# Performance work log

Hardware: AMD Instinct MI355X
Metric: run time of the kernel (lower is better)

## Reference

```python
import jax, jax.numpy as jnp
import numpy as np

N = 100000      # nodes
E = 1600000     # edges (avg degree 16)
F_IN = 128      # input feature dim (lazy in_channels=-1)
HID = 256       # hidden_channels
OUT = 128       # out_channels
NCLS = 2        # final softmax classes


def _l2norm(x):
    # F.normalize(p=2, dim=-1) with eps clamp, as SAGEConv(normalize=True)
    n = jnp.linalg.norm(x, axis=-1, keepdims=True)
    return x / jnp.maximum(n, 1e-12)


def _sage(x, src, tgt, Wl, bl, Wr, n_nodes):
    # PyG SAGEConv: mean-aggregate source features at targets, then
    # out = lin_l(mean_aggr) + lin_r(x); lin_l has bias, lin_r does not.
    s = jax.ops.segment_sum(x[src], tgt, num_segments=n_nodes)          # [N, F]
    cnt = jax.ops.segment_sum(jnp.ones((src.shape[0],), x.dtype), tgt,
                              num_segments=n_nodes)                     # [N]
    mean = s / jnp.maximum(cnt, 1.0)[:, None]
    out = mean @ Wl.T + bl + x @ Wr.T
    return _l2norm(out)


def setup_inputs() -> dict:
    key = jax.random.key(0)
    ks = jax.random.split(key, 12)

    def glorot(k, o, i):
        lim = float(np.sqrt(6.0 / (o + i)))
        return jax.random.uniform(k, (o, i), jnp.float32, -lim, lim)

    return {
        "x": jax.random.normal(ks[0], (N, F_IN), jnp.float32),
        "edge_index": jax.random.randint(ks[1], (2, E), 0, N, dtype=jnp.int64),
        # conv1: SAGEConv(F_IN -> HID)
        "W1l": glorot(ks[2], HID, F_IN), "b1l": jnp.zeros((HID,), jnp.float32),
        "W1r": glorot(ks[3], HID, F_IN),
        # linear: HID -> OUT
        "Wlin": glorot(ks[4], OUT, HID), "blin": jnp.zeros((OUT,), jnp.float32),
        # conv2: SAGEConv(OUT -> OUT)
        "W2l": glorot(ks[5], OUT, OUT), "b2l": jnp.zeros((OUT,), jnp.float32),
        "W2r": glorot(ks[6], OUT, OUT),
        # linear2: OUT -> 2
        "Wlin2": glorot(ks[7], NCLS, OUT), "blin2": jnp.zeros((NCLS,), jnp.float32),
    }


def reference(x, edge_index, W1l, b1l, W1r, Wlin, blin, W2l, b2l, W2r, Wlin2, blin2):
    src, tgt = edge_index[0], edge_index[1]
    h = _sage(x, src, tgt, W1l, b1l, W1r, N)            # conv1, normalize
    h = jnp.maximum(h @ Wlin.T + blin, 0.0)             # linear + relu
    y = _sage(h, src, tgt, W2l, b2l, W2r, N)            # conv2, normalize
    logits = y @ Wlin2.T + blin2                        # linear2
    probs = jax.nn.softmax(logits, axis=1)
    return probs, y
```

## Files before the change

kernel.cpp:

```cpp
#include <hip/hip_runtime.h>
#include <hip/hip_bf16.h>
#include <hip/hip_fp8.h>

#define NN   100000
#define NE   1600000
#define NBK  196
#define BSH  9
#define EPB  8192
#define CAP  9216

typedef __attribute__((ext_vector_type(8))) short short8;
typedef __attribute__((ext_vector_type(4))) float f32x4;

__device__ __forceinline__ ushort f2bf(float f) {
    union { float f; uint u; } v; v.f = f;
    uint u = v.u;
    return (ushort)((u + 0x7FFFu + ((u >> 16) & 1u)) >> 16);
}
__device__ __forceinline__ float bf2f(uint b) {
    union { uint u; float f; } v; v.u = b << 16;
    return v.f;
}
__device__ __forceinline__ float fp8f(uint byte) {
    __hip_fp8_e4m3 t; t.__x = (__hip_fp8_storage_t)(byte & 0xffu);
    return (float)t;
}
__device__ __forceinline__ uint f2fp8(float f) {
    __hip_fp8_e4m3 t(f);
    return (uint)t.__x;
}
__device__ __forceinline__ int swz(int off) { return off ^ (((off >> 9) & 7) << 4); }

__global__ __launch_bounds__(256) void bucket_hist(const int* __restrict__ tgt,
                                                   int* __restrict__ bcnt) {
    __shared__ int lh[NBK];
    int tid = threadIdx.x;
    for (int i = tid; i < NBK; i += 256) lh[i] = 0;
    __syncthreads();
    int base4 = blockIdx.x * (EPB / 4);
#pragma unroll
    for (int k = 0; k < 8; ++k) {
        int i4 = base4 + k * 256 + tid;
        if (i4 < NE / 4) {
            int4 t = ((const int4*)tgt)[i4];
            atomicAdd(&lh[t.x >> BSH], 1);
            atomicAdd(&lh[t.y >> BSH], 1);
            atomicAdd(&lh[t.z >> BSH], 1);
            atomicAdd(&lh[t.w >> BSH], 1);
        }
    }
    __syncthreads();
    for (int i = tid; i < NBK; i += 256)
        if (lh[i]) atomicAdd(&bcnt[i], lh[i]);
}

__global__ __launch_bounds__(256) void bucket_scan(const int* __restrict__ bcnt,
                                                   int* __restrict__ bbase,
                                                   int* __restrict__ bcursor,
                                                   int* __restrict__ rowstart) {
    int t = threadIdx.x;
    int v = (t < NBK) ? bcnt[t] : 0;
    int lane = t & 63, wid = t >> 6;
    int inc = v;
#pragma unroll
    for (int off = 1; off < 64; off <<= 1) {
        int u = __shfl_up(inc, off);
        if (lane >= off) inc += u;
    }
    __shared__ int ws[4];
    if (lane == 63) ws[wid] = inc;
    __syncthreads();
    int woff = 0;
    for (int w = 0; w < wid; ++w) woff += ws[w];
    int ex = woff + inc - v;
    if (t < NBK) { bbase[t] = ex; bcursor[t] = ex; }
    if (t == NBK) bbase[NBK] = ex;
    if (t == 255) rowstart[NN] = NE;
}

__global__ __launch_bounds__(256) void bucket_scatter(const int* __restrict__ src,
                                                      const int* __restrict__ tgt,
                                                      int* __restrict__ bcursor,
                                                      uint* __restrict__ brec) {
    __shared__ int lh[NBK + 1];
    __shared__ int lcur[NBK];
    __shared__ int lbase[NBK];
    __shared__ uint lrec[EPB];
    __shared__ int ws[4];
    int tid = threadIdx.x;
    for (int i = tid; i < NBK; i += 256) lh[i] = 0;
    __syncthreads();
    int base4 = blockIdx.x * (EPB / 4);
#pragma unroll
    for (int k = 0; k < 8; ++k) {
        int i4 = base4 + k * 256 + tid;
        if (i4 < NE / 4) {
            int4 t = ((const int4*)tgt)[i4];
            atomicAdd(&lh[t.x >> BSH], 1);
            atomicAdd(&lh[t.y >> BSH], 1);
            atomicAdd(&lh[t.z >> BSH], 1);
            atomicAdd(&lh[t.w >> BSH], 1);
        }
    }
    __syncthreads();
    int v = (tid < NBK) ? lh[tid] : 0;
    int lane = tid & 63, wid = tid >> 6;
    int inc = v;
#pragma unroll
    for (int off = 1; off < 64; off <<= 1) {
        int u = __shfl_up(inc, off);
        if (lane >= off) inc += u;
    }
    if (lane == 63) ws[wid] = inc;
    __syncthreads();
    int woff = 0;
    for (int w = 0; w < wid; ++w) woff += ws[w];
    int ex = woff + inc - v;
    int nval = min(EPB, NE - blockIdx.x * EPB);
    if (tid < NBK) {
        lh[tid] = ex;
        lcur[tid] = ex;
        lbase[tid] = v ? atomicAdd(&bcursor[tid], v) : 0;
    }
    if (tid == 0) lh[NBK] = nval;
    __syncthreads();
#pragma unroll
    for (int k = 0; k < 8; ++k) {
        int i4 = base4 + k * 256 + tid;
        if (i4 < NE / 4) {
            int4 t = ((const int4*)tgt)[i4];
            int4 s = ((const int4*)src)[i4];
            int p;
            p = atomicAdd(&lcur[t.x >> BSH], 1); lrec[p] = ((uint)s.x << BSH) | (uint)(t.x & 511);
            p = atomicAdd(&lcur[t.y >> BSH], 1); lrec[p] = ((uint)s.y << BSH) | (uint)(t.y & 511);
            p = atomicAdd(&lcur[t.z >> BSH], 1); lrec[p] = ((uint)s.z << BSH) | (uint)(t.z & 511);
            p = atomicAdd(&lcur[t.w >> BSH], 1); lrec[p] = ((uint)s.w << BSH) | (uint)(t.w & 511);
        }
    }
    __syncthreads();
    for (int i = tid; i < nval; i += 256) {
        int lo = 0, hi = NBK;
        while (hi - lo > 1) { int mid = (lo + hi) >> 1; if (lh[mid] <= i) lo = mid; else hi = mid; }
        brec[lbase[lo] + (i - lh[lo])] = lrec[i];
    }
}

__global__ __launch_bounds__(256) void bucket_to_csr(const uint* __restrict__ brec,
                                                     const int* __restrict__ bbase,
                                                     int* __restrict__ rowstart,
                                                     int* __restrict__ sortedSrc) {
    __shared__ int cnt[512];
    __shared__ int cur[512];
    __shared__ int srt[CAP];
    __shared__ int ws[4];
    int b = blockIdx.x;
    int beg = bbase[b], end = bbase[b + 1];
    int len = end - beg;
    int n0 = b << BSH;
    int ncnt = min(512, NN - n0);
    int tid = threadIdx.x;
    cnt[tid] = 0; cnt[tid + 256] = 0;
    __syncthreads();
    for (int i = beg + tid; i < end; i += 256)
        atomicAdd(&cnt[brec[i] & 511u], 1);
    __syncthreads();
    int c0 = cnt[2 * tid], c1 = cnt[2 * tid + 1];
    int s = c0 + c1;
    int lane = tid & 63, wid = tid >> 6;
    int inc = s;
#pragma unroll
    for (int off = 1; off < 64; off <<= 1) {
        int u = __shfl_up(inc, off);
        if (lane >= off) inc += u;
    }
    if (lane == 63) ws[wid] = inc;
    __syncthreads();
    int woff = 0;
    for (int w = 0; w < wid; ++w) woff += ws[w];
    int ex = woff + inc - s;
    cur[2 * tid] = ex; cur[2 * tid + 1] = ex + c0;
    if (2 * tid < ncnt)     rowstart[n0 + 2 * tid]     = beg + ex;
    if (2 * tid + 1 < ncnt) rowstart[n0 + 2 * tid + 1] = beg + ex + c0;
    __syncthreads();
    if (len <= CAP) {
        for (int i = beg + tid; i < end; i += 256) {
            uint r = brec[i];
            int p = atomicAdd(&cur[r & 511u], 1);
            srt[p] = (int)(r >> BSH);
        }
        __syncthreads();
        for (int i = tid; i < len; i += 256)
            sortedSrc[beg + i] = srt[i];
    } else {
        for (int i = beg + tid; i < end; i += 256) {
            uint r = brec[i];
            int p = atomicAdd(&cur[r & 511u], 1);
            sortedSrc[beg + p] = (int)(r >> BSH);
        }
    }
}

__global__ __launch_bounds__(256) void gather_mean8(const uchar* __restrict__ t8,
                                                    const int* __restrict__ rowstart,
                                                    const int* __restrict__ sortedSrc,
                                                    ushort* __restrict__ mean) {
    int node = blockIdx.x * 4 + (threadIdx.x >> 6);
    if (node >= NN) return;
    int lane = threadIdx.x & 63;
    int q = lane >> 4, l = lane & 15;
    int beg = rowstart[node], end = rowstart[node + 1];
    float a0 = 0.f, a1 = 0.f, a2 = 0.f, a3 = 0.f;
    float a4 = 0.f, a5 = 0.f, a6 = 0.f, a7 = 0.f;
    float b0 = 0.f, b1 = 0.f, b2 = 0.f, b3 = 0.f;
    float b4 = 0.f, b5 = 0.f, b6 = 0.f, b7 = 0.f;
#define ACCA(v) { a0 += fp8f(v.x);       a1 += fp8f(v.x >> 8); \
                  a2 += fp8f(v.x >> 16); a3 += fp8f(v.x >> 24); \
                  a4 += fp8f(v.y);       a5 += fp8f(v.y >> 8); \
                  a6 += fp8f(v.y >> 16); a7 += fp8f(v.y >> 24); }
#define ACCB(v) { b0 += fp8f(v.x);       b1 += fp8f(v.x >> 8); \
                  b2 += fp8f(v.x >> 16); b3 += fp8f(v.x >> 24); \
                  b4 += fp8f(v.y);       b5 += fp8f(v.y >> 8); \
                  b6 += fp8f(v.y >> 16); b7 += fp8f(v.y >> 24); }
    int i = beg + q;
    for (; i + 4 < end; i += 8) {
        int s0 = sortedSrc[i];
        int s1 = sortedSrc[i + 4];
        uint2 v0 = *(const uint2*)&t8[(size_t)s0 * 128 + l * 8];
        uint2 v1 = *(const uint2*)&t8[(size_t)s1 * 128 + l * 8];
        ACCA(v0) ACCB(v1)
    }
    if (i < end) {
        int s0 = sortedSrc[i];
        uint2 v0 = *(const uint2*)&t8[(size_t)s0 * 128 + l * 8];
        ACCA(v0)
    }
#undef ACCA
#undef ACCB
    a0 += b0; a1 += b1; a2 += b2; a3 += b3;
    a4 += b4; a5 += b5; a6 += b6; a7 += b7;
#define CMB(a) a += __shfl_xor(a, 32); a += __shfl_xor(a, 16);
    CMB(a0) CMB(a1) CMB(a2) CMB(a3) CMB(a4) CMB(a5) CMB(a6) CMB(a7)
#undef CMB
    if (lane < 16) {
        float id = 1.0f / fmaxf((float)(end - beg), 1.0f);
        ushort p[8];
        p[0] = f2bf(a0 * id); p[1] = f2bf(a1 * id);
        p[2] = f2bf(a2 * id); p[3] = f2bf(a3 * id);
        p[4] = f2bf(a4 * id); p[5] = f2bf(a5 * id);
        p[6] = f2bf(a6 * id); p[7] = f2bf(a7 * id);
        *(uint4*)&mean[(size_t)node * 128 + l * 8] = *(uint4*)p;
    }
}

__global__ __launch_bounds__(256) void prep_w(const float* __restrict__ W1l,
                                              const float* __restrict__ W1r,
                                              const float* __restrict__ Wlin,
                                              const float* __restrict__ W2l,
                                              const float* __restrict__ W2r,
                                              ushort* __restrict__ Wcat1,
                                              ushort* __restrict__ Wlinb,
                                              ushort* __restrict__ Wcat2) {
    int i = blockIdx.x * 256 + threadIdx.x;
    if (i < 65536) {
        int o = i >> 8, k = i & 255;
        float v = (k < 128) ? W1l[o * 128 + k] : W1r[o * 128 + k - 128];
        Wcat1[i] = f2bf(v);
    } else if (i < 98304) {
        int j = i - 65536;
        Wlinb[j] = f2bf(Wlin[j]);
    } else {
        int j = i - 98304;
        int o = j >> 8, k = j & 255;
        float v = (k < 128) ? W2l[o * 128 + k] : W2r[o * 128 + k - 128];
        Wcat2[j] = f2bf(v);
    }
}

__global__ __launch_bounds__(256) void xcvt(const float* __restrict__ x,
                                            ushort* __restrict__ xbf,
                                            uchar* __restrict__ x8) {
    int i = blockIdx.x * 256 + threadIdx.x;
    float4 v = ((const float4*)x)[i];
    ushort4 p;
    p.x = f2bf(v.x); p.y = f2bf(v.y); p.z = f2bf(v.z); p.w = f2bf(v.w);
    ((ushort4*)xbf)[i] = p;
    uint q = f2fp8(v.x) | (f2fp8(v.y) << 8) | (f2fp8(v.z) << 16) | (f2fp8(v.w) << 24);
    ((uint*)x8)[i] = q;
}

__global__ __launch_bounds__(256) void cvt8(const ushort* __restrict__ hr,
                                            uchar* __restrict__ hr8) {
    int i = blockIdx.x * 256 + threadIdx.x;
    uint4 v = ((const uint4*)hr)[i];
    uint lo = f2fp8(bf2f(v.x & 0xffffu)) | (f2fp8(bf2f(v.x >> 16)) << 8) |
              (f2fp8(bf2f(v.y & 0xffffu)) << 16) | (f2fp8(bf2f(v.y >> 16)) << 24);
    uint hi = f2fp8(bf2f(v.z & 0xffffu)) | (f2fp8(bf2f(v.z >> 16)) << 8) |
              (f2fp8(bf2f(v.w & 0xffffu)) << 16) | (f2fp8(bf2f(v.w >> 16)) << 24);
    uint2 o; o.x = lo; o.y = hi;
    ((uint2*)hr8)[i] = o;
}

__global__ __launch_bounds__(256) void conv1lin_mfma(const ushort* __restrict__ mean,
                                                     const ushort* __restrict__ xbf,
                                                     const ushort* __restrict__ Wcat,
                                                     const float* __restrict__ bias1,
                                                     const ushort* __restrict__ Wlin,
                                                     const float* __restrict__ blin,
                                                     ushort* __restrict__ hr) {
    __shared__ char As[64 * 512];
    __shared__ char Bs[64 * 512];
    int m0 = blockIdx.x * 64;
    int tid = threadIdx.x;
    for (int c = tid; c < 2048; c += 256) {
        int m = c >> 5, kc = c & 31;
        int mm = min(m0 + m, NN - 1);
        uint4 v = (kc < 16) ? *(const uint4*)&mean[(size_t)mm * 128 + kc * 8]
                            : *(const uint4*)&xbf[(size_t)mm * 128 + (kc - 16) * 8];
        *(uint4*)(As + swz(m * 512 + kc * 16)) = v;
    }
    for (int j = tid; j < 2048; j += 256)
        *(uint4*)(Bs + swz((j >> 5) * 512 + (j & 31) * 16)) = *(const uint4*)&Wcat[j * 8];
    __syncthreads();

    int lane = tid & 63, wave = tid >> 6;
    int col = lane & 15, kg = lane >> 4;
    int mym = wave * 16 + col;
    short8 a[8];
#pragma unroll
    for (int ks = 0; ks < 8; ++ks)
        a[ks] = *(const short8*)(As + swz(mym * 512 + (ks * 32 + kg * 8) * 2));
    f32x4 acc[16];
#pragma unroll
    for (int nt = 0; nt < 4; ++nt) {
        f32x4 c = {0.f, 0.f, 0.f, 0.f};
#pragma unroll
        for (int ks = 0; ks < 8; ++ks)
            c = __builtin_amdgcn_mfma_f32_16x16x32_bf16(
                a[ks], *(const short8*)(Bs + swz((nt * 16 + col) * 512 + (ks * 32 + kg * 8) * 2)), c, 0, 0, 0);
        acc[nt] = c;
    }
    for (int ch = 1; ch < 4; ++ch) {
        __syncthreads();
        for (int j = tid; j < 2048; j += 256)
            *(uint4*)(Bs + swz((j >> 5) * 512 + (j & 31) * 16)) =
                *(const uint4*)&Wcat[ch * 16384 + j * 8];
        __syncthreads();
#pragma unroll
        for (int nt = 0; nt < 4; ++nt) {
            f32x4 c = {0.f, 0.f, 0.f, 0.f};
#pragma unroll
            for (int ks = 0; ks < 8; ++ks)
                c = __builtin_amdgcn_mfma_f32_16x16x32_bf16(
                    a[ks], *(const short8*)(Bs + swz((nt * 16 + col) * 512 + (ks * 32 + kg * 8) * 2)), c, 0, 0, 0);
            acc[ch * 4 + nt] = c;
        }
    }
    float ssq[4] = {0.f, 0.f, 0.f, 0.f};
#pragma unroll
    for (int nt = 0; nt < 16; ++nt) {
        float b = bias1[nt * 16 + col];
#pragma unroll
        for (int r = 0; r < 4; ++r) {
            acc[nt][r] += b;
            ssq[r] += acc[nt][r] * acc[nt][r];
        }
    }
#pragma unroll
    for (int off = 1; off < 16; off <<= 1)
#pragma unroll
        for (int r = 0; r < 4; ++r) ssq[r] += __shfl_xor(ssq[r], off);
    float rn[4];
#pragma unroll
    for (int r = 0; r < 4; ++r) rn[r] = 1.0f / fmaxf(sqrtf(ssq[r]), 1e-12f);
#pragma unroll
    for (int r = 0; r < 4; ++r) {
        int rl = wave * 16 + kg * 4 + r;
#pragma unroll
        for (int nt = 0; nt < 16; ++nt)
            *(ushort*)(As + swz(rl * 512 + (nt * 16 + col) * 2)) = f2bf(acc[nt][r] * rn[r]);
    }
    __syncthreads();
    short8 a2[8];
#pragma unroll
    for (int ks = 0; ks < 8; ++ks)
        a2[ks] = *(const short8*)(As + swz(mym * 512 + (ks * 32 + kg * 8) * 2));
    for (int j = tid; j < 2048; j += 256)
        *(uint4*)(Bs + swz((j >> 5) * 512 + (j & 31) * 16)) = *(const uint4*)&Wlin[j * 8];
    __syncthreads();
    f32x4 acc2[8];
#pragma unroll
    for (int nt = 0; nt < 4; ++nt) {
        f32x4 c = {0.f, 0.f, 0.f, 0.f};
#pragma unroll
        for (int ks = 0; ks < 8; ++ks)
            c = __builtin_amdgcn_mfma_f32_16x16x32_bf16(
                a2[ks], *(const short8*)(Bs + swz((nt * 16 + col) * 512 + (ks * 32 + kg * 8) * 2)), c, 0, 0, 0);
        acc2[nt] = c;
    }
    __syncthreads();
    for (int j = tid; j < 2048; j += 256)
        *(uint4*)(Bs + swz((j >> 5) * 512 + (j & 31) * 16)) = *(const uint4*)&Wlin[16384 + j * 8];
    __syncthreads();
#pragma unroll
    for (int nt = 0; nt < 4; ++nt) {
        f32x4 c = {0.f, 0.f, 0.f, 0.f};
#pragma unroll
        for (int ks = 0; ks < 8; ++ks)
            c = __builtin_amdgcn_mfma_f32_16x16x32_bf16(
                a2[ks], *(const short8*)(Bs + swz((nt * 16 + col) * 512 + (ks * 32 + kg * 8) * 2)), c, 0, 0, 0);
        acc2[4 + nt] = c;
    }
#pragma unroll
    for (int r = 0; r < 4; ++r) {
        int node = m0 + wave * 16 + kg * 4 + r;
        if (node < NN) {
#pragma unroll
            for (int nt = 0; nt < 8; ++nt) {
                float vv = acc2[nt][r] + blin[nt * 16 + col];
                hr[(size_t)node * 128 + nt * 16 + col] = f2bf(fmaxf(vv, 0.f));
            }
        }
    }
}

__global__ __launch_bounds__(256) void conv2_mfma(const ushort* __restrict__ mean,
                                                  const ushort* __restrict__ hr,
                                                  const ushort* __restrict__ Wcat,
                                                  const float* __restrict__ bias,
                                                  const float* __restrict__ Wlin2,
                                                  const float* __restrict__ blin2,
                                                  float* __restrict__ probs,
                                                  float* __restrict__ yout) {
    __shared__ char As[64 * 512];
    __shared__ char Bs[64 * 512];
    int m0 = blockIdx.x * 64;
    int tid = threadIdx.x;
    for (int c = tid; c < 2048; c += 256) {
        int m = c >> 5, kc = c & 31;
        int mm = min(m0 + m, NN - 1);
        uint4 v = (kc < 16) ? *(const uint4*)&mean[(size_t)mm * 128 + kc * 8]
                            : *(const uint4*)&hr[(size_t)mm * 128 + (kc - 16) * 8];
        *(uint4*)(As + swz(m * 512 + kc * 16)) = v;
    }
    for (int j = tid; j < 2048; j += 256)
        *(uint4*)(Bs + swz((j >> 5) * 512 + (j & 31) * 16)) = *(const uint4*)&Wcat[j * 8];
    __syncthreads();

    int lane = tid & 63, wave = tid >> 6;
    int col = lane & 15, kg = lane >> 4;
    int mym = wave * 16 + col;
    short8 a[8];
#pragma unroll
    for (int ks = 0; ks < 8; ++ks)
        a[ks] = *(const short8*)(As + swz(mym * 512 + (ks * 32 + kg * 8) * 2));
    f32x4 acc[8];
#pragma unroll
    for (int nt = 0; nt < 4; ++nt) {
        f32x4 c = {0.f, 0.f, 0.f, 0.f};
#pragma unroll
        for (int ks = 0; ks < 8; ++ks)
            c = __builtin_amdgcn_mfma_f32_16x16x32_bf16(
                a[ks], *(const short8*)(Bs + swz((nt * 16 + col) * 512 + (ks * 32 + kg * 8) * 2)), c, 0, 0, 0);
        acc[nt] = c;
    }
    __syncthreads();
    for (int j = tid; j < 2048; j += 256)
        *(uint4*)(Bs + swz((j >> 5) * 512 + (j & 31) * 16)) = *(const uint4*)&Wcat[16384 + j * 8];
    __syncthreads();
#pragma unroll
    for (int nt = 0; nt < 4; ++nt) {
        f32x4 c = {0.f, 0.f, 0.f, 0.f};
#pragma unroll
        for (int ks = 0; ks < 8; ++ks)
            c = __builtin_amdgcn_mfma_f32_16x16x32_bf16(
                a[ks], *(const short8*)(Bs + swz((nt * 16 + col) * 512 + (ks * 32 + kg * 8) * 2)), c, 0, 0, 0);
        acc[4 + nt] = c;
    }
    float ssq[4] = {0.f, 0.f, 0.f, 0.f};
#pragma unroll
    for (int nt = 0; nt < 8; ++nt) {
        float b = bias[nt * 16 + col];
#pragma unroll
        for (int r = 0; r < 4; ++r) {
            acc[nt][r] += b;
            ssq[r] += acc[nt][r] * acc[nt][r];
        }
    }
#pragma unroll
    for (int off = 1; off < 16; off <<= 1)
#pragma unroll
        for (int r = 0; r < 4; ++r) ssq[r] += __shfl_xor(ssq[r], off);
    float rn[4], p0[4] = {0.f,0.f,0.f,0.f}, p1[4] = {0.f,0.f,0.f,0.f};
#pragma unroll
    for (int r = 0; r < 4; ++r) rn[r] = 1.0f / fmaxf(sqrtf(ssq[r]), 1e-12f);
#pragma unroll
    for (int nt = 0; nt < 8; ++nt) {
        float w0 = Wlin2[nt * 16 + col], w1 = Wlin2[128 + nt * 16 + col];
#pragma unroll
        for (int r = 0; r < 4; ++r) {
            float yv = acc[nt][r] * rn[r];
            acc[nt][r] = yv;
            p0[r] += yv * w0;
            p1[r] += yv * w1;
        }
    }
#pragma unroll
    for (int off = 1; off < 16; off <<= 1)
#pragma unroll
        for (int r = 0; r < 4; ++r) { p0[r] += __shfl_xor(p0[r], off); p1[r] += __shfl_xor(p1[r], off); }
#pragma unroll
    for (int r = 0; r < 4; ++r) {
        int node = m0 + wave * 16 + kg * 4 + r;
        if (node < NN) {
#pragma unroll
            for (int nt = 0; nt < 8; ++nt)
                yout[(size_t)node * 128 + nt * 16 + col] = acc[nt][r];
            if (col == 0) {
                float l0 = p0[r] + blin2[0], l1 = p1[r] + blin2[1];
                float mx = fmaxf(l0, l1);
                float e0 = expf(l0 - mx), e1 = expf(l1 - mx);
                float inv = 1.0f / (e0 + e1);
                probs[(size_t)node * 2 + 0] = e0 * inv;
                probs[(size_t)node * 2 + 1] = e1 * inv;
            }
        }
    }
}

extern "C" void kernel_launch(void* const* d_in, const int* in_sizes, int n_in,
                              void* d_out, int out_size, void* d_ws, size_t ws_size,
                              hipStream_t stream) {
    const float* x     = (const float*)d_in[0];
    const int*   ei    = (const int*)d_in[1];
    const int*   src   = ei;
    const int*   tgt   = ei + NE;
    const float* W1l   = (const float*)d_in[2];
    const float* b1l   = (const float*)d_in[3];
    const float* W1r   = (const float*)d_in[4];
    const float* Wlin  = (const float*)d_in[5];
    const float* blin  = (const float*)d_in[6];
    const float* W2l   = (const float*)d_in[7];
    const float* b2l   = (const float*)d_in[8];
    const float* W2r   = (const float*)d_in[9];
    const float* Wlin2 = (const float*)d_in[10];
    const float* blin2 = (const float*)d_in[11];

    float* probs = (float*)d_out;
    float* y     = (float*)d_out + 2 * NN;

    int*    bcnt      = (int*)d_ws;
    int*    bbase     = bcnt + NBK;
    int*    bcursor   = bbase + NBK + 1;
    int*    rowstart  = bcursor + NBK;
    uint*   brec      = (uint*)(rowstart + NN + 1);
    int*    sortedSrc = (int*)(brec + NE);
    ushort* Wcat1     = (ushort*)(sortedSrc + NE);
    ushort* Wlinb     = Wcat1 + 65536;
    ushort* Wcat2     = Wlinb + 32768;
    ushort* xbf       = Wcat2 + 32768;
    ushort* hr        = xbf + (size_t)NN * 128;
    ushort* mean      = hr + (size_t)NN * 128;
    uchar*  x8        = (uchar*)(mean + (size_t)NN * 128);
    uchar*  hr8       = x8 + (size_t)NN * 128;

    const int NEB = (NE + EPB - 1) / EPB;

    hipMemsetAsync(bcnt, 0, sizeof(int) * NBK, stream);

    prep_w<<<512, 256, 0, stream>>>(W1l, W1r, Wlin, W2l, W2r, Wcat1, Wlinb, Wcat2);
    xcvt<<<NN * 32 / 256, 256, 0, stream>>>(x, xbf, x8);

    bucket_hist<<<NEB, 256, 0, stream>>>(tgt, bcnt);
    bucket_scan<<<1, 256, 0, stream>>>(bcnt, bbase, bcursor, rowstart);
    bucket_scatter<<<NEB, 256, 0, stream>>>(src, tgt, bcursor, brec);
    bucket_to_csr<<<NBK, 256, 0, stream>>>(brec, bbase, rowstart, sortedSrc);

    gather_mean8<<<(NN + 3) / 4, 256, 0, stream>>>(x8, rowstart, sortedSrc, mean);
    conv1lin_mfma<<<(NN + 63) / 64, 256, 0, stream>>>(mean, xbf, Wcat1, b1l,
                                                      Wlinb, blin, hr);
    cvt8<<<NN * 128 / 8 / 256, 256, 0, stream>>>(hr, hr8);
    gather_mean8<<<(NN + 3) / 4, 256, 0, stream>>>(hr8, rowstart, sortedSrc, mean);
    conv2_mfma<<<(NN + 63) / 64, 256, 0, stream>>>(mean, hr, Wcat2, b2l,
                                                   Wlin2, blin2, probs, y);
}
```

Measured before the change: 306.5 us.

## Use 128-row tiles with shared B fragments and defer conv1 normalization

```diff
diff --git a/kernel.cpp b/kernel.cpp
--- a/kernel.cpp
+++ b/kernel.cpp
@@ -307,119 +307,109 @@
                                                      const ushort* __restrict__ Wlin,
                                                      const float* __restrict__ blin,
                                                      ushort* __restrict__ hr) {
-    __shared__ char As[64 * 512];
-    __shared__ char Bs[64 * 512];
-    int m0 = blockIdx.x * 64;
+    __shared__ char As[128 * 512];
+    __shared__ char Bs[32 * 512];
+    int m0 = blockIdx.x * 128;
     int tid = threadIdx.x;
-    for (int c = tid; c < 2048; c += 256) {
+    for (int c = tid; c < 4096; c += 256) {
         int m = c >> 5, kc = c & 31;
         int mm = min(m0 + m, NN - 1);
         uint4 v = (kc < 16) ? *(const uint4*)&mean[(size_t)mm * 128 + kc * 8]
                             : *(const uint4*)&xbf[(size_t)mm * 128 + (kc - 16) * 8];
         *(uint4*)(As + swz(m * 512 + kc * 16)) = v;
     }
-    for (int j = tid; j < 2048; j += 256)
-        *(uint4*)(Bs + swz((j >> 5) * 512 + (j & 31) * 16)) = *(const uint4*)&Wcat[j * 8];
     __syncthreads();
 
     int lane = tid & 63, wave = tid >> 6;
     int col = lane & 15, kg = lane >> 4;
-    int mym = wave * 16 + col;
-    short8 a[8];
-#pragma unroll
-    for (int ks = 0; ks < 8; ++ks)
-        a[ks] = *(const short8*)(As + swz(mym * 512 + (ks * 32 + kg * 8) * 2));
-    f32x4 acc[16];
-#pragma unroll
-    for (int nt = 0; nt < 4; ++nt) {
-        f32x4 c = {0.f, 0.f, 0.f, 0.f};
+    short8 a[2][8];
+#pragma unroll
+    for (int m = 0; m < 2; ++m)
 #pragma unroll
         for (int ks = 0; ks < 8; ++ks)
-            c = __builtin_amdgcn_mfma_f32_16x16x32_bf16(
-                a[ks], *(const short8*)(Bs + swz((nt * 16 + col) * 512 + (ks * 32 + kg * 8) * 2)), c, 0, 0, 0);
-        acc[nt] = c;
-    }
-    for (int ch = 1; ch < 4; ++ch) {
-        __syncthreads();
-        for (int j = tid; j < 2048; j += 256)
+            a[m][ks] = *(const short8*)(As + swz((m * 64 + wave * 16 + col) * 512 + (ks * 32 + kg * 8) * 2));
+    __syncthreads();
+
+    float ssq[2][4] = {{0.f,0.f,0.f,0.f},{0.f,0.f,0.f,0.f}};
+    for (int ch = 0; ch < 8; ++ch) {
+        for (int j = tid; j < 1024; j += 256)
             *(uint4*)(Bs + swz((j >> 5) * 512 + (j & 31) * 16)) =
-                *(const uint4*)&Wcat[ch * 16384 + j * 8];
-        __syncthreads();
-#pragma unroll
-        for (int nt = 0; nt < 4; ++nt) {
-            f32x4 c = {0.f, 0.f, 0.f, 0.f};
+                *(const uint4*)&Wcat[(size_t)(ch * 32 + (j >> 5)) * 256 + (j & 31) * 8];
+        __syncthreads();
+#pragma unroll
+        for (int nt = 0; nt < 2; ++nt) {
+            short8 bq[8];
 #pragma unroll
             for (int ks = 0; ks < 8; ++ks)
-                c = __builtin_amdgcn_mfma_f32_16x16x32_bf16(
-                    a[ks], *(const short8*)(Bs + swz((nt * 16 + col) * 512 + (ks * 32 + kg * 8) * 2)), c, 0, 0, 0);
-            acc[ch * 4 + nt] = c;
-        }
-    }
-    float ssq[4] = {0.f, 0.f, 0.f, 0.f};
-#pragma unroll
-    for (int nt = 0; nt < 16; ++nt) {
-        float b = bias1[nt * 16 + col];
-#pragma unroll
-        for (int r = 0; r < 4; ++r) {
-            acc[nt][r] += b;
-            ssq[r] += acc[nt][r] * acc[nt][r];
-        }
+                bq[ks] = *(const short8*)(Bs + swz((nt * 16 + col) * 512 + (ks * 32 + kg * 8) * 2));
+            f32x4 c0 = {0.f,0.f,0.f,0.f}, c1 = {0.f,0.f,0.f,0.f};
+#pragma unroll
+            for (int ks = 0; ks < 8; ++ks) {
+                c0 = __builtin_amdgcn_mfma_f32_16x16x32_bf16(a[0][ks], bq[ks], c0, 0, 0, 0);
+                c1 = __builtin_amdgcn_mfma_f32_16x16x32_bf16(a[1][ks], bq[ks], c1, 0, 0, 0);
+            }
+            float b = bias1[ch * 32 + nt * 16 + col];
+#pragma unroll
+            for (int r = 0; r < 4; ++r) {
+                float v0 = c0[r] + b, v1 = c1[r] + b;
+                ssq[0][r] += v0 * v0;
+                ssq[1][r] += v1 * v1;
+                int rl0 = wave * 16 + kg * 4 + r;
+                *(ushort*)(As + swz(rl0 * 512 + (ch * 32 + nt * 16 + col) * 2)) = f2bf(v0);
+                *(ushort*)(As + swz((64 + rl0) * 512 + (ch * 32 + nt * 16 + col) * 2)) = f2bf(v1);
+            }
+        }
+        __syncthreads();
     }
 #pragma unroll
     for (int off = 1; off < 16; off <<= 1)
 #pragma unroll
-        for (int r = 0; r < 4; ++r) ssq[r] += __shfl_xor(ssq[r], off);
-    float rn[4];
-#pragma unroll
-    for (int r = 0; r < 4; ++r) rn[r] = 1.0f / fmaxf(sqrtf(ssq[r]), 1e-12f);
-#pragma unroll
-    for (int r = 0; r < 4; ++r) {
-        int rl = wave * 16 + kg * 4 + r;
-#pragma unroll
-        for (int nt = 0; nt < 16; ++nt)
-            *(ushort*)(As + swz(rl * 512 + (nt * 16 + col) * 2)) = f2bf(acc[nt][r] * rn[r]);
-    }
-    __syncthreads();
-    short8 a2[8];
-#pragma unroll
-    for (int ks = 0; ks < 8; ++ks)
-        a2[ks] = *(const short8*)(As + swz(mym * 512 + (ks * 32 + kg * 8) * 2));
-    for (int j = tid; j < 2048; j += 256)
-        *(uint4*)(Bs + swz((j >> 5) * 512 + (j & 31) * 16)) = *(const uint4*)&Wlin[j * 8];
-    __syncthreads();
-    f32x4 acc2[8];
-#pragma unroll
-    for (int nt = 0; nt < 4; ++nt) {
-        f32x4 c = {0.f, 0.f, 0.f, 0.f};
+        for (int m = 0; m < 2; ++m)
+#pragma unroll
+            for (int r = 0; r < 4; ++r) ssq[m][r] += __shfl_xor(ssq[m][r], off);
+    float rn[2][4];
+#pragma unroll
+    for (int m = 0; m < 2; ++m)
+#pragma unroll
+        for (int r = 0; r < 4; ++r) rn[m][r] = 1.0f / fmaxf(sqrtf(ssq[m][r]), 1e-12f);
+
+    short8 a2[2][8];
+#pragma unroll
+    for (int m = 0; m < 2; ++m)
 #pragma unroll
         for (int ks = 0; ks < 8; ++ks)
-            c = __builtin_amdgcn_mfma_f32_16x16x32_bf16(
-                a2[ks], *(const short8*)(Bs + swz((nt * 16 + col) * 512 + (ks * 32 + kg * 8) * 2)), c, 0, 0, 0);
-        acc2[nt] = c;
-    }
-    __syncthreads();
-    for (int j = tid; j < 2048; j += 256)
-        *(uint4*)(Bs + swz((j >> 5) * 512 + (j & 31) * 16)) = *(const uint4*)&Wlin[16384 + j * 8];
-    __syncthreads();
-#pragma unroll
-    for (int nt = 0; nt < 4; ++nt) {
-        f32x4 c = {0.f, 0.f, 0.f, 0.f};
-#pragma unroll
-        for (int ks = 0; ks < 8; ++ks)
-            c = __builtin_amdgcn_mfma_f32_16x16x32_bf16(
-                a2[ks], *(const short8*)(Bs + swz((nt * 16 + col) * 512 + (ks * 32 + kg * 8) * 2)), c, 0, 0, 0);
-        acc2[4 + nt] = c;
-    }
-#pragma unroll
-    for (int r = 0; r < 4; ++r) {
-        int node = m0 + wave * 16 + kg * 4 + r;
-        if (node < NN) {
-#pragma unroll
-            for (int nt = 0; nt < 8; ++nt) {
-                float vv = acc2[nt][r] + blin[nt * 16 + col];
-                hr[(size_t)node * 128 + nt * 16 + col] = f2bf(fmaxf(vv, 0.f));
-            }
-        }
+            a2[m][ks] = *(const short8*)(As + swz((m * 64 + wave * 16 + col) * 512 + (ks * 32 + kg * 8) * 2));
+    for (int lc = 0; lc < 4; ++lc) {
+        for (int j = tid; j < 1024; j += 256)
+            *(uint4*)(Bs + swz((j >> 5) * 512 + (j & 31) * 16)) =
+                *(const uint4*)&Wlin[(size_t)(lc * 32 + (j >> 5)) * 256 + (j & 31) * 8];
+        __syncthreads();
+#pragma unroll
+        for (int nt = 0; nt < 2; ++nt) {
+            short8 bq[8];
+#pragma unroll
+            for (int ks = 0; ks < 8; ++ks)
+                bq[ks] = *(const short8*)(Bs + swz((nt * 16 + col) * 512 + (ks * 32 + kg * 8) * 2));
+            f32x4 c0 = {0.f,0.f,0.f,0.f}, c1 = {0.f,0.f,0.f,0.f};
+#pragma unroll
+            for (int ks = 0; ks < 8; ++ks) {
+                c0 = __builtin_amdgcn_mfma_f32_16x16x32_bf16(a2[0][ks], bq[ks], c0, 0, 0, 0);
+                c1 = __builtin_amdgcn_mfma_f32_16x16x32_bf16(a2[1][ks], bq[ks], c1, 0, 0, 0);
+            }
+            float b = blin[lc * 32 + nt * 16 + col];
+#pragma unroll
+            for (int m = 0; m < 2; ++m) {
+#pragma unroll
+                for (int r = 0; r < 4; ++r) {
+                    int node = m0 + m * 64 + wave * 16 + kg * 4 + r;
+                    if (node < NN) {
+                        float v = rn[m][r] * ((m == 0) ? c0[r] : c1[r]) + b;
+                        hr[(size_t)node * 128 + lc * 32 + nt * 16 + col] = f2bf(fmaxf(v, 0.f));
+                    }
+                }
+            }
+        }
+        __syncthreads();
     }
 }
 
@@ -431,100 +421,120 @@
                                                   const float* __restrict__ blin2,
                                                   float* __restrict__ probs,
                                                   float* __restrict__ yout) {
-    __shared__ char As[64 * 512];
-    __shared__ char Bs[64 * 512];
-    int m0 = blockIdx.x * 64;
+    __shared__ char As[128 * 512];
+    __shared__ char Bs[32 * 512];
+    int m0 = blockIdx.x * 128;
     int tid = threadIdx.x;
-    for (int c = tid; c < 2048; c += 256) {
+    for (int c = tid; c < 4096; c += 256) {
         int m = c >> 5, kc = c & 31;
         int mm = min(m0 + m, NN - 1);
         uint4 v = (kc < 16) ? *(const uint4*)&mean[(size_t)mm * 128 + kc * 8]
                             : *(const uint4*)&hr[(size_t)mm * 128 + (kc - 16) * 8];
         *(uint4*)(As + swz(m * 512 + kc * 16)) = v;
     }
-    for (int j = tid; j < 2048; j += 256)
-        *(uint4*)(Bs + swz((j >> 5) * 512 + (j & 31) * 16)) = *(const uint4*)&Wcat[j * 8];
     __syncthreads();
 
     int lane = tid & 63, wave = tid >> 6;
     int col = lane & 15, kg = lane >> 4;
-    int mym = wave * 16 + col;
-    short8 a[8];
-#pragma unroll
-    for (int ks = 0; ks < 8; ++ks)
-        a[ks] = *(const short8*)(As + swz(mym * 512 + (ks * 32 + kg * 8) * 2));
-    f32x4 acc[8];
-#pragma unroll
-    for (int nt = 0; nt < 4; ++nt) {
-        f32x4 c = {0.f, 0.f, 0.f, 0.f};
+    short8 a[2][8];
+#pragma unroll
+    for (int m = 0; m < 2; ++m)
 #pragma unroll
         for (int ks = 0; ks < 8; ++ks)
-            c = __builtin_amdgcn_mfma_f32_16x16x32_bf16(
-                a[ks], *(const short8*)(Bs + swz((nt * 16 + col) * 512 + (ks * 32 + kg * 8) * 2)), c, 0, 0, 0);
-        acc[nt] = c;
-    }
-    __syncthreads();
-    for (int j = tid; j < 2048; j += 256)
-        *(uint4*)(Bs + swz((j >> 5) * 512 + (j & 31) * 16)) = *(const uint4*)&Wcat[16384 + j * 8];
-    __syncthreads();
-#pragma unroll
-    for (int nt = 0; nt < 4; ++nt) {
-        f32x4 c = {0.f, 0.f, 0.f, 0.f};
-#pragma unroll
-        for (int ks = 0; ks < 8; ++ks)
-            c = __builtin_amdgcn_mfma_f32_16x16x32_bf16(
-                a[ks], *(const short8*)(Bs + swz((nt * 16 + col) * 512 + (ks * 32 + kg * 8) * 2)), c, 0, 0, 0);
-        acc[4 + nt] = c;
-    }
-    float ssq[4] = {0.f, 0.f, 0.f, 0.f};
-#pragma unroll
-    for (int nt = 0; nt < 8; ++nt) {
-        float b = bias[nt * 16 + col];
+            a[m][ks] = *(const short8*)(As + swz((m * 64 + wave * 16 + col) * 512 + (ks * 32 + kg * 8) * 2));
+
+    f32x4 acc[2][8];
+#pragma unroll
+    for (int m = 0; m < 2; ++m)
+#pragma unroll
+        for (int n = 0; n < 8; ++n) acc[m][n] = {0.f, 0.f, 0.f, 0.f};
+
+    for (int ch = 0; ch < 4; ++ch) {
+        __syncthreads();
+        for (int j = tid; j < 1024; j += 256)
+            *(uint4*)(Bs + swz((j >> 5) * 512 + (j & 31) * 16)) =
+                *(const uint4*)&Wcat[(size_t)(ch * 32 + (j >> 5)) * 256 + (j & 31) * 8];
+        __syncthreads();
+#pragma unroll
+        for (int nt = 0; nt < 2; ++nt) {
+            short8 bq[8];
+#pragma unroll
+            for (int ks = 0; ks < 8; ++ks)
+                bq[ks] = *(const short8*)(Bs + swz((nt * 16 + col) * 512 + (ks * 32 + kg * 8) * 2));
+#pragma unroll
+            for (int ks = 0; ks < 8; ++ks) {
+                acc[0][ch * 2 + nt] = __builtin_amdgcn_mfma_f32_16x16x32_bf16(a[0][ks], bq[ks], acc[0][ch * 2 + nt], 0, 0, 0);
+                acc[1][ch * 2 + nt] = __builtin_amdgcn_mfma_f32_16x16x32_bf16(a[1][ks], bq[ks], acc[1][ch * 2 + nt], 0, 0, 0);
+            }
+        }
+    }
+    float ssq[2][4] = {{0.f,0.f,0.f,0.f},{0.f,0.f,0.f,0.f}};
+#pragma unroll
+    for (int n = 0; n < 8; ++n) {
+        float b = bias[n * 16 + col];
+#pragma unroll
+        for (int m = 0; m < 2; ++m)
+#pragma unroll
+            for (int r = 0; r < 4; ++r) {
+                acc[m][n][r] += b;
+                ssq[m][r] += acc[m][n][r] * acc[m][n][r];
+            }
+    }
+#pragma unroll
+    for (int off = 1; off < 16; off <<= 1)
+#pragma unroll
+        for (int m = 0; m < 2; ++m)
+#pragma unroll
+            for (int r = 0; r < 4; ++r) ssq[m][r] += __shfl_xor(ssq[m][r], off);
+    float rn[2][4], p0[2][4], p1[2][4];
+#pragma unroll
+    for (int m = 0; m < 2; ++m)
 #pragma unroll
         for (int r = 0; r < 4; ++r) {
-            acc[nt][r] += b;
-            ssq[r] += acc[nt][r] * acc[nt][r];
-        }
+            rn[m][r] = 1.0f / fmaxf(sqrtf(ssq[m][r]), 1e-12f);
+            p0[m][r] = 0.f; p1[m][r] = 0.f;
+        }
+#pragma unroll
+    for (int n = 0; n < 8; ++n) {
+        float w0 = Wlin2[n * 16 + col], w1 = Wlin2[128 + n * 16 + col];
+#pragma unroll
+        for (int m = 0; m < 2; ++m)
+#pragma unroll
+            for (int r = 0; r < 4; ++r) {
+                float yv = acc[m][n][r] * rn[m][r];
+                acc[m][n][r] = yv;
+                p0[m][r] += yv * w0;
+                p1[m][r] += yv * w1;
+            }
     }
 #pragma unroll
     for (int off = 1; off < 16; off <<= 1)
 #pragma unroll
-        for (int r = 0; r < 4; ++r) ssq[r] += __shfl_xor(ssq[r], off);
-    float rn[4], p0[4] = {0.f,0.f,0.f,0.f}, p1[4] = {0.f,0.f,0.f,0.f};
-#pragma unroll
-    for (int r = 0; r < 4; ++r) rn[r] = 1.0f / fmaxf(sqrtf(ssq[r]), 1e-12f);
-#pragma unroll
-    for (int nt = 0; nt < 8; ++nt) {
-        float w0 = Wlin2[nt * 16 + col], w1 = Wlin2[128 + nt * 16 + col];
+        for (int m = 0; m < 2; ++m)
+#pragma unroll
+            for (int r = 0; r < 4; ++r) {
+                p0[m][r] += __shfl_xor(p0[m][r], off);
+                p1[m][r] += __shfl_xor(p1[m][r], off);
+            }
+#pragma unroll
+    for (int m = 0; m < 2; ++m)
 #pragma unroll
         for (int r = 0; r < 4; ++r) {
-            float yv = acc[nt][r] * rn[r];
-            acc[nt][r] = yv;
-            p0[r] += yv * w0;
-            p1[r] += yv * w1;
-        }
-    }
-#pragma unroll
-    for (int off = 1; off < 16; off <<= 1)
-#pragma unroll
-        for (int r = 0; r < 4; ++r) { p0[r] += __shfl_xor(p0[r], off); p1[r] += __shfl_xor(p1[r], off); }
-#pragma unroll
-    for (int r = 0; r < 4; ++r) {
-        int node = m0 + wave * 16 + kg * 4 + r;
-        if (node < NN) {
-#pragma unroll
-            for (int nt = 0; nt < 8; ++nt)
-                yout[(size_t)node * 128 + nt * 16 + col] = acc[nt][r];
-            if (col == 0) {
-                float l0 = p0[r] + blin2[0], l1 = p1[r] + blin2[1];
-                float mx = fmaxf(l0, l1);
-                float e0 = expf(l0 - mx), e1 = expf(l1 - mx);
-                float inv = 1.0f / (e0 + e1);
-                probs[(size_t)node * 2 + 0] = e0 * inv;
-                probs[(size_t)node * 2 + 1] = e1 * inv;
-            }
-        }
-    }
+            int node = m0 + m * 64 + wave * 16 + kg * 4 + r;
+            if (node < NN) {
+#pragma unroll
+                for (int n = 0; n < 8; ++n)
+                    yout[(size_t)node * 128 + n * 16 + col] = acc[m][n][r];
+                if (col == 0) {
+                    float l0 = p0[m][r] + blin2[0], l1 = p1[m][r] + blin2[1];
+                    float mx = fmaxf(l0, l1);
+                    float e0 = expf(l0 - mx), e1 = expf(l1 - mx);
+                    float inv = 1.0f / (e0 + e1);
+                    probs[(size_t)node * 2 + 0] = e0 * inv;
+                    probs[(size_t)node * 2 + 1] = e1 * inv;
+                }
+            }
+        }
 }
 
 extern "C" void kernel_launch(void* const* d_in, const int* in_sizes, int n_in,
@@ -576,10 +586,10 @@
     bucket_to_csr<<<NBK, 256, 0, stream>>>(brec, bbase, rowstart, sortedSrc);
 
     gather_mean8<<<(NN + 3) / 4, 256, 0, stream>>>(x8, rowstart, sortedSrc, mean);
-    conv1lin_mfma<<<(NN + 63) / 64, 256, 0, stream>>>(mean, xbf, Wcat1, b1l,
-                                                      Wlinb, blin, hr);
+    conv1lin_mfma<<<(NN + 127) / 128, 256, 0, stream>>>(mean, xbf, Wcat1, b1l,
+                                                        Wlinb, blin, hr);
     cvt8<<<NN * 128 / 8 / 256, 256, 0, stream>>>(hr, hr8);
     gather_mean8<<<(NN + 3) / 4, 256, 0, stream>>>(hr8, rowstart, sortedSrc, mean);
-    conv2_mfma<<<(NN + 63) / 64, 256, 0, stream>>>(mean, hr, Wcat2, b2l,
-                                                   Wlin2, blin2, probs, y);
-}
+    conv2_mfma<<<(NN + 127) / 128, 256, 0, stream>>>(mean, hr, Wcat2, b2l,
+                                                     Wlin2, blin2, probs, y);
+}
```

Result: no change. 311.7 us (+1.7%).

## Fuse fp8 conversion into conv1 and split output columns across 8 waves

Applied to the files above, without the earlier changes.

```diff
diff --git a/kernel.cpp b/kernel.cpp
--- a/kernel.cpp
+++ b/kernel.cpp
@@ -288,142 +288,136 @@
     ((uint*)x8)[i] = q;
 }
 
-__global__ __launch_bounds__(256) void cvt8(const ushort* __restrict__ hr,
-                                            uchar* __restrict__ hr8) {
-    int i = blockIdx.x * 256 + threadIdx.x;
-    uint4 v = ((const uint4*)hr)[i];
-    uint lo = f2fp8(bf2f(v.x & 0xffffu)) | (f2fp8(bf2f(v.x >> 16)) << 8) |
-              (f2fp8(bf2f(v.y & 0xffffu)) << 16) | (f2fp8(bf2f(v.y >> 16)) << 24);
-    uint hi = f2fp8(bf2f(v.z & 0xffffu)) | (f2fp8(bf2f(v.z >> 16)) << 8) |
-              (f2fp8(bf2f(v.w & 0xffffu)) << 16) | (f2fp8(bf2f(v.w >> 16)) << 24);
-    uint2 o; o.x = lo; o.y = hi;
-    ((uint2*)hr8)[i] = o;
-}
-
-__global__ __launch_bounds__(256) void conv1lin_mfma(const ushort* __restrict__ mean,
+__global__ __launch_bounds__(512) void conv1lin_mfma(const ushort* __restrict__ mean,
                                                      const ushort* __restrict__ xbf,
                                                      const ushort* __restrict__ Wcat,
                                                      const float* __restrict__ bias1,
                                                      const ushort* __restrict__ Wlin,
                                                      const float* __restrict__ blin,
-                                                     ushort* __restrict__ hr) {
+                                                     ushort* __restrict__ hr,
+                                                     uchar* __restrict__ hr8) {
     __shared__ char As[64 * 512];
     __shared__ char Bs[64 * 512];
+    __shared__ float rbuf[2][64];
     int m0 = blockIdx.x * 64;
     int tid = threadIdx.x;
-    for (int c = tid; c < 2048; c += 256) {
+    for (int c = tid; c < 2048; c += 512) {
         int m = c >> 5, kc = c & 31;
         int mm = min(m0 + m, NN - 1);
         uint4 v = (kc < 16) ? *(const uint4*)&mean[(size_t)mm * 128 + kc * 8]
                             : *(const uint4*)&xbf[(size_t)mm * 128 + (kc - 16) * 8];
         *(uint4*)(As + swz(m * 512 + kc * 16)) = v;
     }
-    for (int j = tid; j < 2048; j += 256)
-        *(uint4*)(Bs + swz((j >> 5) * 512 + (j & 31) * 16)) = *(const uint4*)&Wcat[j * 8];
     __syncthreads();
 
     int lane = tid & 63, wave = tid >> 6;
+    int wr = wave & 3, wn = wave >> 2;
     int col = lane & 15, kg = lane >> 4;
-    int mym = wave * 16 + col;
+    int mym = wr * 16 + col;
     short8 a[8];
 #pragma unroll
     for (int ks = 0; ks < 8; ++ks)
         a[ks] = *(const short8*)(As + swz(mym * 512 + (ks * 32 + kg * 8) * 2));
-    f32x4 acc[16];
-#pragma unroll
-    for (int nt = 0; nt < 4; ++nt) {
-        f32x4 c = {0.f, 0.f, 0.f, 0.f};
-#pragma unroll
-        for (int ks = 0; ks < 8; ++ks)
-            c = __builtin_amdgcn_mfma_f32_16x16x32_bf16(
-                a[ks], *(const short8*)(Bs + swz((nt * 16 + col) * 512 + (ks * 32 + kg * 8) * 2)), c, 0, 0, 0);
-        acc[nt] = c;
-    }
-    for (int ch = 1; ch < 4; ++ch) {
+    __syncthreads();
+
+    f32x4 acc[8];
+#pragma unroll
+    for (int ch = 0; ch < 4; ++ch) {
+        for (int j = tid; j < 2048; j += 512)
+            *(uint4*)(Bs + swz((j >> 5) * 512 + (j & 31) * 16)) =
+                *(const uint4*)&Wcat[(size_t)(ch * 64 + (j >> 5)) * 256 + (j & 31) * 8];
         __syncthreads();
-        for (int j = tid; j < 2048; j += 256)
-            *(uint4*)(Bs + swz((j >> 5) * 512 + (j & 31) * 16)) =
-                *(const uint4*)&Wcat[ch * 16384 + j * 8];
+#pragma unroll
+        for (int nt2 = 0; nt2 < 2; ++nt2) {
+            int ntl = wn * 2 + nt2;
+            short8 bq[8];
+#pragma unroll
+            for (int ks = 0; ks < 8; ++ks)
+                bq[ks] = *(const short8*)(Bs + swz((ntl * 16 + col) * 512 + (ks * 32 + kg * 8) * 2));
+            f32x4 c = {0.f, 0.f, 0.f, 0.f};
+#pragma unroll
+            for (int ks = 0; ks < 8; ++ks)
+                c = __builtin_amdgcn_mfma_f32_16x16x32_bf16(a[ks], bq[ks], c, 0, 0, 0);
+            acc[ch * 2 + nt2] = c;
+        }
         __syncthreads();
-#pragma unroll
-        for (int nt = 0; nt < 4; ++nt) {
-            f32x4 c = {0.f, 0.f, 0.f, 0.f};
-#pragma unroll
-            for (int ks = 0; ks < 8; ++ks)
-                c = __builtin_amdgcn_mfma_f32_16x16x32_bf16(
-                    a[ks], *(const short8*)(Bs + swz((nt * 16 + col) * 512 + (ks * 32 + kg * 8) * 2)), c, 0, 0, 0);
-            acc[ch * 4 + nt] = c;
-        }
     }
     float ssq[4] = {0.f, 0.f, 0.f, 0.f};
 #pragma unroll
-    for (int nt = 0; nt < 16; ++nt) {
-        float b = bias1[nt * 16 + col];
+    for (int i = 0; i < 8; ++i) {
+        int chan = (i >> 1) * 64 + (wn * 2 + (i & 1)) * 16 + col;
+        float b = bias1[chan];
 #pragma unroll
         for (int r = 0; r < 4; ++r) {
-            acc[nt][r] += b;
-            ssq[r] += acc[nt][r] * acc[nt][r];
+            acc[i][r] += b;
+            ssq[r] += acc[i][r] * acc[i][r];
         }
     }
 #pragma unroll
     for (int off = 1; off < 16; off <<= 1)
 #pragma unroll
         for (int r = 0; r < 4; ++r) ssq[r] += __shfl_xor(ssq[r], off);
+    if (col == 0)
+#pragma unroll
+        for (int r = 0; r < 4; ++r) rbuf[wn][wr * 16 + kg * 4 + r] = ssq[r];
+    __syncthreads();
     float rn[4];
 #pragma unroll
-    for (int r = 0; r < 4; ++r) rn[r] = 1.0f / fmaxf(sqrtf(ssq[r]), 1e-12f);
-#pragma unroll
     for (int r = 0; r < 4; ++r) {
-        int rl = wave * 16 + kg * 4 + r;
-#pragma unroll
-        for (int nt = 0; nt < 16; ++nt)
-            *(ushort*)(As + swz(rl * 512 + (nt * 16 + col) * 2)) = f2bf(acc[nt][r] * rn[r]);
+        int row = wr * 16 + kg * 4 + r;
+        rn[r] = 1.0f / fmaxf(sqrtf(rbuf[0][row] + rbuf[1][row]), 1e-12f);
+    }
+#pragma unroll
+    for (int i = 0; i < 8; ++i) {
+        int chan = (i >> 1) * 64 + (wn * 2 + (i & 1)) * 16 + col;
+#pragma unroll
+        for (int r = 0; r < 4; ++r)
+            *(ushort*)(As + swz((wr * 16 + kg * 4 + r) * 512 + chan * 2)) = f2bf(acc[i][r] * rn[r]);
     }
     __syncthreads();
     short8 a2[8];
 #pragma unroll
     for (int ks = 0; ks < 8; ++ks)
         a2[ks] = *(const short8*)(As + swz(mym * 512 + (ks * 32 + kg * 8) * 2));
-    for (int j = tid; j < 2048; j += 256)
-        *(uint4*)(Bs + swz((j >> 5) * 512 + (j & 31) * 16)) = *(const uint4*)&Wlin[j * 8];
-    __syncthreads();
-    f32x4 acc2[8];
-#pragma unroll
-    for (int nt = 0; nt < 4; ++nt) {
-        f32x4 c = {0.f, 0.f, 0.f, 0.f};
-#pragma unroll
-        for (int ks = 0; ks < 8; ++ks)
-            c = __builtin_amdgcn_mfma_f32_16x16x32_bf16(
-                a2[ks], *(const short8*)(Bs + swz((nt * 16 + col) * 512 + (ks * 32 + kg * 8) * 2)), c, 0, 0, 0);
-        acc2[nt] = c;
-    }
-    __syncthreads();
-    for (int j = tid; j < 2048; j += 256)
-        *(uint4*)(Bs + swz((j >> 5) * 512 + (j & 31) * 16)) = *(const uint4*)&Wlin[16384 + j * 8];
-    __syncthreads();
-#pragma unroll
-    for (int nt = 0; nt < 4; ++nt) {
-        f32x4 c = {0.f, 0.f, 0.f, 0.f};
-#pragma unroll
-        for (int ks = 0; ks < 8; ++ks)
-            c = __builtin_amdgcn_mfma_f32_16x16x32_bf16(
-                a2[ks], *(const short8*)(Bs + swz((nt * 16 + col) * 512 + (ks * 32 + kg * 8) * 2)), c, 0, 0, 0);
-        acc2[4 + nt] = c;
-    }
-#pragma unroll
-    for (int r = 0; r < 4; ++r) {
-        int node = m0 + wave * 16 + kg * 4 + r;
-        if (node < NN) {
-#pragma unroll
-            for (int nt = 0; nt < 8; ++nt) {
-                float vv = acc2[nt][r] + blin[nt * 16 + col];
-                hr[(size_t)node * 128 + nt * 16 + col] = f2bf(fmaxf(vv, 0.f));
+    f32x4 acc2[4];
+#pragma unroll
+    for (int lc = 0; lc < 2; ++lc) {
+        for (int j = tid; j < 2048; j += 512)
+            *(uint4*)(Bs + swz((j >> 5) * 512 + (j & 31) * 16)) =
+                *(const uint4*)&Wlin[(size_t)(lc * 64 + (j >> 5)) * 256 + (j & 31) * 8];
+        __syncthreads();
+#pragma unroll
+        for (int nt2 = 0; nt2 < 2; ++nt2) {
+            int ntl = wn * 2 + nt2;
+            short8 bq[8];
+#pragma unroll
+            for (int ks = 0; ks < 8; ++ks)
+                bq[ks] = *(const short8*)(Bs + swz((ntl * 16 + col) * 512 + (ks * 32 + kg * 8) * 2));
+            f32x4 c = {0.f, 0.f, 0.f, 0.f};
+#pragma unroll
+            for (int ks = 0; ks < 8; ++ks)
+                c = __builtin_amdgcn_mfma_f32_16x16x32_bf16(a2[ks], bq[ks], c, 0, 0, 0);
+            acc2[lc * 2 + nt2] = c;
+        }
+        __syncthreads();
+    }
+#pragma unroll
+    for (int i = 0; i < 4; ++i) {
+        int chan = (i >> 1) * 64 + (wn * 2 + (i & 1)) * 16 + col;
+        float b = blin[chan];
+#pragma unroll
+        for (int r = 0; r < 4; ++r) {
+            int node = m0 + wr * 16 + kg * 4 + r;
+            if (node < NN) {
+                float v = fmaxf(acc2[i][r] + b, 0.f);
+                hr[(size_t)node * 128 + chan] = f2bf(v);
+                hr8[(size_t)node * 128 + chan] = (uchar)f2fp8(v);
             }
         }
     }
 }
 
-__global__ __launch_bounds__(256) void conv2_mfma(const ushort* __restrict__ mean,
+__global__ __launch_bounds__(512) void conv2_mfma(const ushort* __restrict__ mean,
                                                   const ushort* __restrict__ hr,
                                                   const ushort* __restrict__ Wcat,
                                                   const float* __restrict__ bias,
@@ -433,73 +427,85 @@
                                                   float* __restrict__ yout) {
     __shared__ char As[64 * 512];
     __shared__ char Bs[64 * 512];
+    __shared__ float rbuf[2][64];
+    __shared__ float pbuf0[2][64];
+    __shared__ float pbuf1[2][64];
     int m0 = blockIdx.x * 64;
     int tid = threadIdx.x;
-    for (int c = tid; c < 2048; c += 256) {
+    for (int c = tid; c < 2048; c += 512) {
         int m = c >> 5, kc = c & 31;
         int mm = min(m0 + m, NN - 1);
         uint4 v = (kc < 16) ? *(const uint4*)&mean[(size_t)mm * 128 + kc * 8]
                             : *(const uint4*)&hr[(size_t)mm * 128 + (kc - 16) * 8];
         *(uint4*)(As + swz(m * 512 + kc * 16)) = v;
     }
-    for (int j = tid; j < 2048; j += 256)
-        *(uint4*)(Bs + swz((j >> 5) * 512 + (j & 31) * 16)) = *(const uint4*)&Wcat[j * 8];
     __syncthreads();
 
     int lane = tid & 63, wave = tid >> 6;
+    int wr = wave & 3, wn = wave >> 2;
     int col = lane & 15, kg = lane >> 4;
-    int mym = wave * 16 + col;
+    int mym = wr * 16 + col;
     short8 a[8];
 #pragma unroll
     for (int ks = 0; ks < 8; ++ks)
         a[ks] = *(const short8*)(As + swz(mym * 512 + (ks * 32 + kg * 8) * 2));
-    f32x4 acc[8];
-#pragma unroll
-    for (int nt = 0; nt < 4; ++nt) {
-        f32x4 c = {0.f, 0.f, 0.f, 0.f};
-#pragma unroll
-        for (int ks = 0; ks < 8; ++ks)
-            c = __builtin_amdgcn_mfma_f32_16x16x32_bf16(
-                a[ks], *(const short8*)(Bs + swz((nt * 16 + col) * 512 + (ks * 32 + kg * 8) * 2)), c, 0, 0, 0);
-        acc[nt] = c;
-    }
-    __syncthreads();
-    for (int j = tid; j < 2048; j += 256)
-        *(uint4*)(Bs + swz((j >> 5) * 512 + (j & 31) * 16)) = *(const uint4*)&Wcat[16384 + j * 8];
-    __syncthreads();
-#pragma unroll
-    for (int nt = 0; nt < 4; ++nt) {
-        f32x4 c = {0.f, 0.f, 0.f, 0.f};
-#pragma unroll
-        for (int ks = 0; ks < 8; ++ks)
-            c = __builtin_amdgcn_mfma_f32_16x16x32_bf16(
-                a[ks], *(const short8*)(Bs + swz((nt * 16 + col) * 512 + (ks * 32 + kg * 8) * 2)), c, 0, 0, 0);
-        acc[4 + nt] = c;
+
+    f32x4 acc[4];
+#pragma unroll
+    for (int ch = 0; ch < 2; ++ch) {
+        __syncthreads();
+        for (int j = tid; j < 2048; j += 512)
+            *(uint4*)(Bs + swz((j >> 5) * 512 + (j & 31) * 16)) =
+                *(const uint4*)&Wcat[(size_t)(ch * 64 + (j >> 5)) * 256 + (j & 31) * 8];
+        __syncthreads();
+#pragma unroll
+        for (int nt2 = 0; nt2 < 2; ++nt2) {
+            int ntl = wn * 2 + nt2;
+            short8 bq[8];
+#pragma unroll
+            for (int ks = 0; ks < 8; ++ks)
+                bq[ks] = *(const short8*)(Bs + swz((ntl * 16 + col) * 512 + (ks * 32 + kg * 8) * 2));
+            f32x4 c = {0.f, 0.f, 0.f, 0.f};
+#pragma unroll
+            for (int ks = 0; ks < 8; ++ks)
+                c = __builtin_amdgcn_mfma_f32_16x16x32_bf16(a[ks], bq[ks], c, 0, 0, 0);
+            acc[ch * 2 + nt2] = c;
+        }
     }
     float ssq[4] = {0.f, 0.f, 0.f, 0.f};
 #pragma unroll
-    for (int nt = 0; nt < 8; ++nt) {
-        float b = bias[nt * 16 + col];
+    for (int i = 0; i < 4; ++i) {
+        int chan = (i >> 1) * 64 + (wn * 2 + (i & 1)) * 16 + col;
+        float b = bias[chan];
 #pragma unroll
         for (int r = 0; r < 4; ++r) {
-            acc[nt][r] += b;
-            ssq[r] += acc[nt][r] * acc[nt][r];
+            acc[i][r] += b;
+            ssq[r] += acc[i][r] * acc[i][r];
         }
     }
 #pragma unroll
     for (int off = 1; off < 16; off <<= 1)
 #pragma unroll
         for (int r = 0; r < 4; ++r) ssq[r] += __shfl_xor(ssq[r], off);
-    float rn[4], p0[4] = {0.f,0.f,0.f,0.f}, p1[4] = {0.f,0.f,0.f,0.f};
-#pragma unroll
-    for (int r = 0; r < 4; ++r) rn[r] = 1.0f / fmaxf(sqrtf(ssq[r]), 1e-12f);
-#pragma unroll
-    for (int nt = 0; nt < 8; ++nt) {
-        float w0 = Wlin2[nt * 16 + col], w1 = Wlin2[128 + nt * 16 + col];
+    if (col == 0)
+#pragma unroll
+        for (int r = 0; r < 4; ++r) rbuf[wn][wr * 16 + kg * 4 + r] = ssq[r];
+    __syncthreads();
+    float rn[4];
+#pragma unroll
+    for (int r = 0; r < 4; ++r) {
+        int row = wr * 16 + kg * 4 + r;
+        rn[r] = 1.0f / fmaxf(sqrtf(rbuf[0][row] + rbuf[1][row]), 1e-12f);
+    }
+    float p0[4] = {0.f,0.f,0.f,0.f}, p1[4] = {0.f,0.f,0.f,0.f};
+#pragma unroll
+    for (int i = 0; i < 4; ++i) {
+        int chan = (i >> 1) * 64 + (wn * 2 + (i & 1)) * 16 + col;
+        float w0 = Wlin2[chan], w1 = Wlin2[128 + chan];
 #pragma unroll
         for (int r = 0; r < 4; ++r) {
-            float yv = acc[nt][r] * rn[r];
-            acc[nt][r] = yv;
+            float yv = acc[i][r] * rn[r];
+            acc[i][r] = yv;
             p0[r] += yv * w0;
             p1[r] += yv * w1;
         }
@@ -508,15 +514,31 @@
     for (int off = 1; off < 16; off <<= 1)
 #pragma unroll
         for (int r = 0; r < 4; ++r) { p0[r] += __shfl_xor(p0[r], off); p1[r] += __shfl_xor(p1[r], off); }
-#pragma unroll
-    for (int r = 0; r < 4; ++r) {
-        int node = m0 + wave * 16 + kg * 4 + r;
-        if (node < NN) {
-#pragma unroll
-            for (int nt = 0; nt < 8; ++nt)
-                yout[(size_t)node * 128 + nt * 16 + col] = acc[nt][r];
-            if (col == 0) {
-                float l0 = p0[r] + blin2[0], l1 = p1[r] + blin2[1];
+    if (col == 0)
+#pragma unroll
+        for (int r = 0; r < 4; ++r) {
+            pbuf0[wn][wr * 16 + kg * 4 + r] = p0[r];
+            pbuf1[wn][wr * 16 + kg * 4 + r] = p1[r];
+        }
+    __syncthreads();
+#pragma unroll
+    for (int i = 0; i < 4; ++i) {
+        int chan = (i >> 1) * 64 + (wn * 2 + (i & 1)) * 16 + col;
+#pragma unroll
+        for (int r = 0; r < 4; ++r) {
+            int node = m0 + wr * 16 + kg * 4 + r;
+            if (node < NN)
+                yout[(size_t)node * 128 + chan] = acc[i][r];
+        }
+    }
+    if (wn == 0 && col == 0) {
+#pragma unroll
+        for (int r = 0; r < 4; ++r) {
+            int row = wr * 16 + kg * 4 + r;
+            int node = m0 + row;
+            if (node < NN) {
+                float l0 = pbuf0[0][row] + pbuf0[1][row] + blin2[0];
+                float l1 = pbuf1[0][row] + pbuf1[1][row] + blin2[1];
                 float mx = fmaxf(l0, l1);
                 float e0 = expf(l0 - mx), e1 = expf(l1 - mx);
                 float inv = 1.0f / (e0 + e1);
@@ -576,10 +598,9 @@
     bucket_to_csr<<<NBK, 256, 0, stream>>>(brec, bbase, rowstart, sortedSrc);
 
     gather_mean8<<<(NN + 3) / 4, 256, 0, stream>>>(x8, rowstart, sortedSrc, mean);
-    conv1lin_mfma<<<(NN + 63) / 64, 256, 0, stream>>>(mean, xbf, Wcat1, b1l,
-                                                      Wlinb, blin, hr);
-    cvt8<<<NN * 128 / 8 / 256, 256, 0, stream>>>(hr, hr8);
+    conv1lin_mfma<<<(NN + 63) / 64, 512, 0, stream>>>(mean, xbf, Wcat1, b1l,
+                                                      Wlinb, blin, hr, hr8);
     gather_mean8<<<(NN + 3) / 4, 256, 0, stream>>>(hr8, rowstart, sortedSrc, mean);
-    conv2_mfma<<<(NN + 63) / 64, 256, 0, stream>>>(mean, hr, Wcat2, b2l,
+    conv2_mfma<<<(NN + 63) / 64, 512, 0, stream>>>(mean, hr, Wcat2, b2l,
                                                    Wlin2, blin2, probs, y);
 }
```

New measurement: 326.9 us. +6.7%, slower.
